# Kernel tuning notes

Hardware: AMD Instinct MI355X
Metric: run time of the kernel (lower is better)

## Reference

```python
import jax, jax.numpy as jnp
import numpy as np

EMBED = 1024
HEADS = 16

def setup_inputs() -> dict:
    key = jax.random.key(0)
    ks = jax.random.split(key, 6)
    N, S = 1, 4096
    half = EMBED // 2
    x = jax.random.normal(ks[0], (N, S, EMBED), dtype=jnp.float32)
    Wq = jax.random.normal(ks[1], (half, half), dtype=jnp.float32) * 0.02
    Wk = jax.random.normal(ks[2], (half, half), dtype=jnp.float32) * 0.02
    Wv = jax.random.normal(ks[3], (half, half), dtype=jnp.float32) * 0.02
    Wo = jax.random.normal(ks[4], (EMBED, half), dtype=jnp.float32) * 0.02
    bo = jnp.zeros((EMBED,), dtype=jnp.float32)
    return {"x": x, "Wq": Wq, "Wk": Wk, "Wv": Wv, "Wo": Wo, "bo": bo}

def reference(x, Wq, Wk, Wv, Wo, bo):
    N, S, E = x.shape
    H = HEADS
    Dh = (E // 2) // H                 # per-head dim of the half-width projections (32)
    scale = float(E // H) ** 0.5       # original scales by head_dim = embed/heads = 64
    left = x[..., : E // 2]            # only the left chunk feeds attention in the source
    # torch Linear: y = x @ W.T (no bias)
    q = (left @ Wq.T).reshape(N, S, H, Dh)
    k = (left @ Wk.T).reshape(N, S, H, Dh)
    v = (left @ Wv.T).reshape(N, S, H, Dh)
    energy = jnp.einsum('nqhd,nkhd->nqkh', q, k)          # [N,S,S,H] full score tensor
    att = jax.nn.softmax(energy / scale, axis=2)          # softmax over key axis
    out = jnp.einsum('nqkh,nkhd->nqhd', att, v)           # [N,S,H,Dh]
    out = out.reshape(N, S, E // 2)
    return out @ Wo.T + bo                                # fc_out: half -> embed
```

## Files before the change

kernel.cpp:

```cpp
#include <hip/hip_runtime.h>
#include <stdint.h>


#define SEQ    4096
#define DMODEL 1024
#define DHALF  512
#define NH     16
#define DH     32

typedef __attribute__((ext_vector_type(4))) float facc4;
typedef __attribute__((ext_vector_type(8))) short bfrag8;

#define MFMA_BF16(a, b, c) __builtin_amdgcn_mfma_f32_16x16x32_bf16((a), (b), (c), 0, 0, 0)

static __device__ __forceinline__ void gll16(const void* g, void* l) {
    typedef const __attribute__((address_space(1))) void GV;
    typedef __attribute__((address_space(3))) void LV;
    __builtin_amdgcn_global_load_lds((GV*)g, (LV*)l, 16, 0, 0);
}

static __device__ __forceinline__ uint16_t f2b(float x) {
    uint32_t u = __float_as_uint(x);
    return (uint16_t)((u + 0x7FFFu + ((u >> 16) & 1u)) >> 16);
}
static __device__ __forceinline__ float b2f(uint16_t b) {
    return __uint_as_float(((uint32_t)b) << 16);
}

static __device__ __forceinline__ bfrag8 cvt8perm(float4 a, float4 b) {
    uint32_t u0 = __float_as_uint(a.x) + 0x8000u, u1 = __float_as_uint(a.y) + 0x8000u;
    uint32_t u2 = __float_as_uint(a.z) + 0x8000u, u3 = __float_as_uint(a.w) + 0x8000u;
    uint32_t u4 = __float_as_uint(b.x) + 0x8000u, u5 = __float_as_uint(b.y) + 0x8000u;
    uint32_t u6 = __float_as_uint(b.z) + 0x8000u, u7 = __float_as_uint(b.w) + 0x8000u;
    union { uint32_t w[4]; bfrag8 r; } u;
    u.w[0] = __builtin_amdgcn_perm(u1, u0, 0x07060302u);
    u.w[1] = __builtin_amdgcn_perm(u3, u2, 0x07060302u);
    u.w[2] = __builtin_amdgcn_perm(u5, u4, 0x07060302u);
    u.w[3] = __builtin_amdgcn_perm(u7, u6, 0x07060302u);
    return u.r;
}

__global__ __launch_bounds__(256) void convert_w(
    const float* __restrict__ Wq, const float* __restrict__ Wk,
    const float* __restrict__ Wv, const float* __restrict__ Wo,
    const float* __restrict__ x,
    uint16_t* __restrict__ q, uint16_t* __restrict__ k,
    uint16_t* __restrict__ v, uint16_t* __restrict__ o,
    uint16_t* __restrict__ xb)
{
    int zz = blockIdx.x;
    if (zz >= 640) {
        size_t g = (size_t)(zz - 640) * 2048 + (size_t)threadIdx.x * 8;
        int row = (int)(g >> 9);
        int col = (int)(g & 511);
        const float* src = &x[(size_t)row * DMODEL + col];
        float4 a = *(const float4*)src;
        float4 b = *(const float4*)(src + 4);
        *(bfrag8*)&xb[g] = cvt8perm(a, b);
        return;
    }
    const float* src; uint16_t* dst; size_t off;
    if      (zz < 128) { src = Wq; dst = q; off = (size_t)zz * 2048; }
    else if (zz < 256) { src = Wk; dst = k; off = (size_t)(zz - 128) * 2048; }
    else if (zz < 384) { src = Wv; dst = v; off = (size_t)(zz - 256) * 2048; }
    else               { src = Wo; dst = o; off = (size_t)(zz - 384) * 2048; }
    size_t i = off + (size_t)threadIdx.x * 8;
    float4 a = *(const float4*)&src[i];
    float4 b = *(const float4*)&src[i + 4];
    *(bfrag8*)&dst[i] = cvt8perm(a, b);
}

__device__ __forceinline__ void gemm128(
    const uint16_t* __restrict__ A, int lda,
    const uint16_t* __restrict__ B, int ldb,
    void* __restrict__ C, int ldc, int cF32,
    const float* __restrict__ bias, float scale,
    int Kd, int m0, int n0)
{
    __shared__ __align__(16) uint16_t As[2][128 * 32];
    __shared__ __align__(16) uint16_t Bs[2][128 * 32];

    const int tid  = threadIdx.x;
    const int lane = tid & 63;
    const int wv   = tid >> 6;
    const int lo   = lane & 15;
    const int quad = lane >> 4;
    const int rb   = (wv >> 1) * 64;
    const int cb   = (wv & 1) * 64;

    const facc4 ZACC = {0.f, 0.f, 0.f, 0.f};
    facc4 acc[4][4];
#pragma unroll
    for (int i = 0; i < 4; ++i)
#pragma unroll
        for (int j = 0; j < 4; ++j) acc[i][j] = ZACC;

    const int lrow = lane >> 2;
    const int scol = (((lane & 3) ^ (lrow & 3)) << 3);
    const uint16_t* gA0 = &A[(size_t)(m0 + wv * 32 + lrow) * lda + scol];
    const uint16_t* gA1 = gA0 + (size_t)16 * lda;
    const uint16_t* gB0 = &B[(size_t)(n0 + wv * 32 + lrow) * ldb + scol];
    const uint16_t* gB1 = gB0 + (size_t)16 * ldb;
    const int d0 = wv * 1024;
    const int d1 = d0 + 512;

    const int rdo = lo * 32 + ((quad ^ (lo & 3)) << 3);

    gll16(gA0, &As[0][d0]); gll16(gA1, &As[0][d1]);
    gll16(gB0, &Bs[0][d0]); gll16(gB1, &Bs[0][d1]);
    __syncthreads();

    int p = 0;
    for (int kt = 0; kt < Kd; kt += 32) {
        const bool more = (kt + 32 < Kd);
        if (more) {
            gll16(gA0 + kt + 32, &As[1 - p][d0]); gll16(gA1 + kt + 32, &As[1 - p][d1]);
            gll16(gB0 + kt + 32, &Bs[1 - p][d0]); gll16(gB1 + kt + 32, &Bs[1 - p][d1]);
        }

        bfrag8 af[4], bf[4];
#pragma unroll
        for (int i = 0; i < 4; ++i) {
            af[i] = *(const bfrag8*)&As[p][rb * 32 + i * 512 + rdo];
            bf[i] = *(const bfrag8*)&Bs[p][cb * 32 + i * 512 + rdo];
        }
#pragma unroll
        for (int i = 0; i < 4; ++i)
#pragma unroll
            for (int j = 0; j < 4; ++j)
                acc[i][j] = MFMA_BF16(bf[j], af[i], acc[i][j]);

        if (more) {
            __syncthreads();
            p ^= 1;
        }
    }

#pragma unroll
    for (int i = 0; i < 4; ++i) {
        const size_t row = (size_t)(m0 + rb + i * 16 + lo);
#pragma unroll
        for (int j = 0; j < 4; ++j) {
            const int colb = n0 + cb + j * 16 + quad * 4;
            float4 bv = {0.f, 0.f, 0.f, 0.f};
            if (bias) bv = *(const float4*)&bias[colb];
            float v0 = acc[i][j][0] * scale + bv.x;
            float v1 = acc[i][j][1] * scale + bv.y;
            float v2 = acc[i][j][2] * scale + bv.z;
            float v3 = acc[i][j][3] * scale + bv.w;
            if (cF32) {
                float4 o = {v0, v1, v2, v3};
                *(float4*)&((float*)C)[row * ldc + colb] = o;
            } else {
                uint2 o;
                o.x = (uint32_t)f2b(v0) | ((uint32_t)f2b(v1) << 16);
                o.y = (uint32_t)f2b(v2) | ((uint32_t)f2b(v3) << 16);
                *(uint2*)&((uint16_t*)C)[row * ldc + colb] = o;
            }
        }
    }
}

#define SC_Q (0.125f * 1.4426950408889634f)

__global__ __launch_bounds__(256, 2) void qkv_kernel(
    const uint16_t* __restrict__ xb,
    const uint16_t* __restrict__ Wqb, const uint16_t* __restrict__ Wkb,
    const uint16_t* __restrict__ Wvb,
    uint16_t* __restrict__ Q, uint16_t* __restrict__ K, uint16_t* __restrict__ V)
{
    const int z = blockIdx.z;
    const uint16_t* W = (z == 0) ? Wqb : (z == 1) ? Wkb : Wvb;
    uint16_t* Out     = (z == 0) ? Q   : (z == 1) ? K   : V;
    float scale       = (z == 0) ? SC_Q : 1.0f;
    gemm128(xb, DHALF, W, DHALF, Out, DHALF, 0, nullptr, scale, DHALF,
            blockIdx.y * 128, blockIdx.x * 128);
}

__global__ __launch_bounds__(256, 2) void outproj_kernel(
    const uint16_t* __restrict__ O, const uint16_t* __restrict__ Wob,
    const float* __restrict__ bo, float* __restrict__ Y)
{
    gemm128(O, DHALF, Wob, DHALF, Y, DMODEL, 1, bo, 1.0f, DHALF,
            blockIdx.y * 128, blockIdx.x * 128);
}

__global__ __launch_bounds__(512) void attn_kernel(
    const uint16_t* __restrict__ Q, const uint16_t* __restrict__ Kb,
    const uint16_t* __restrict__ Vb, uint16_t* __restrict__ Op,
    float* __restrict__ lbuf, int kspan)
{
    __shared__ __align__(16) uint16_t Ks[2][128 * 40];
    __shared__ __align__(16) uint16_t Vt[2][32 * 128];

    const int tid  = threadIdx.x;
    const int lane = tid & 63;
    const int wv   = tid >> 6;
    const int lo   = lane & 15;
    const int quad = lane >> 4;

    const int f  = blockIdx.x + 16 * blockIdx.y + 256 * blockIdx.z;
    const int pp = (f & 7) | ((f >> 7) << 3);
    const int h  = pp & 15;
    const int sp = pp >> 4;
    const int q0 = ((f >> 3) & 15) * 256;

    const int srow = tid >> 2;
    const int skq  = (tid & 3) * 8;

    const facc4 ZACC = {0.f, 0.f, 0.f, 0.f};

    bfrag8 qf[2];
    qf[0] = *(const bfrag8*)&Q[(size_t)(q0 + wv * 32 + lo) * DHALF + h * DH + quad * 8];
    qf[1] = *(const bfrag8*)&Q[(size_t)(q0 + wv * 32 + 16 + lo) * DHALF + h * DH + quad * 8];

    bfrag8 ones;
#pragma unroll
    for (int j = 0; j < 8; ++j) ones[j] = (short)0x3F80;

    int vt_w[8];
    {
        int pb = ((srow >> 5) << 2) | ((srow >> 2) & 3);
        int pw = (((srow >> 4) & 1) << 2) | (srow & 3);
#pragma unroll
        for (int j = 0; j < 8; ++j) {
            int d  = skq + j;
            int Rd = ((d & 7) + 2 * (d >> 3)) & 7;
            vt_w[j] = d * 128 + (((pb + Rd) & 15) << 3) + pw;
        }
    }
    int vt_r[4][2];
#pragma unroll
    for (int dt = 0; dt < 2; ++dt) {
        int d  = dt * 16 + lo;
        int Rd = ((d & 7) + 2 * (d >> 3)) & 7;
#pragma unroll
        for (int c = 0; c < 4; ++c)
            vt_r[c][dt] = d * 128 + ((((c * 4 + quad) + Rd) & 15) << 3);
    }
    const int ks_r = lo * 40 + quad * 8;

    const uint16_t* kp = &Kb[(size_t)(sp * kspan + srow) * DHALF + h * DH + skq];
    const uint16_t* vp = &Vb[(size_t)(sp * kspan + srow) * DHALF + h * DH + skq];

    facc4 oacc[2][2], oaccL[2];
    oacc[0][0] = ZACC; oacc[0][1] = ZACC;
    oacc[1][0] = ZACC; oacc[1][1] = ZACC;
    oaccL[0] = ZACC; oaccL[1] = ZACC;

    float4 kreg = *(const float4*)kp;
    float4 vreg = *(const float4*)vp;
    kp += 128 * DHALF;
    vp += 128 * DHALF;

#define STAGE(BUF) do {                                                       \
        *(float4*)&Ks[BUF][srow * 40 + skq] = kreg;                           \
        const uint16_t* vsp = (const uint16_t*)&vreg;                         \
        _Pragma("unroll")                                                     \
        for (int j = 0; j < 8; ++j) Vt[BUF][vt_w[j]] = vsp[j];                \
    } while (0)

#define HALF(BUF, HH) do {                                                    \
        uint2 w0[4], w1[4];                                                   \
        _Pragma("unroll")                                                     \
        for (int t4 = 0; t4 < 4; ++t4) {                                      \
            bfrag8 kf = *(const bfrag8*)&Ks[BUF][(4 * HH + t4) * 640 + ks_r]; \
            facc4 s0 = MFMA_BF16(kf, qf[0], ZACC);                            \
            facc4 s1 = MFMA_BF16(kf, qf[1], ZACC);                            \
            uint32_t a0 = __float_as_uint(__builtin_amdgcn_exp2f(s0[0])) + 0x8000u; \
            uint32_t a1 = __float_as_uint(__builtin_amdgcn_exp2f(s0[1])) + 0x8000u; \
            uint32_t a2 = __float_as_uint(__builtin_amdgcn_exp2f(s0[2])) + 0x8000u; \
            uint32_t a3 = __float_as_uint(__builtin_amdgcn_exp2f(s0[3])) + 0x8000u; \
            w0[t4].x = __builtin_amdgcn_perm(a1, a0, 0x07060302u);            \
            w0[t4].y = __builtin_amdgcn_perm(a3, a2, 0x07060302u);            \
            uint32_t b0 = __float_as_uint(__builtin_amdgcn_exp2f(s1[0])) + 0x8000u; \
            uint32_t b1 = __float_as_uint(__builtin_amdgcn_exp2f(s1[1])) + 0x8000u; \
            uint32_t b2 = __float_as_uint(__builtin_amdgcn_exp2f(s1[2])) + 0x8000u; \
            uint32_t b3 = __float_as_uint(__builtin_amdgcn_exp2f(s1[3])) + 0x8000u; \
            w1[t4].x = __builtin_amdgcn_perm(b1, b0, 0x07060302u);            \
            w1[t4].y = __builtin_amdgcn_perm(b3, b2, 0x07060302u);            \
        }                                                                     \
        union PU { uint2 u2[2]; bfrag8 f; } pu;                               \
        bfrag8 pf0[2], pf1[2];                                                \
        pu.u2[0] = w0[0]; pu.u2[1] = w0[1]; pf0[0] = pu.f;                    \
        pu.u2[0] = w0[2]; pu.u2[1] = w0[3]; pf0[1] = pu.f;                    \
        pu.u2[0] = w1[0]; pu.u2[1] = w1[1]; pf1[0] = pu.f;                    \
        pu.u2[0] = w1[2]; pu.u2[1] = w1[3]; pf1[1] = pu.f;                    \
        _Pragma("unroll")                                                     \
        for (int cc = 0; cc < 2; ++cc) {                                      \
            _Pragma("unroll")                                                 \
            for (int dt = 0; dt < 2; ++dt) {                                  \
                bfrag8 vf = *(const bfrag8*)&Vt[BUF][vt_r[2 * HH + cc][dt]];  \
                oacc[0][dt] = MFMA_BF16(pf0[cc], vf, oacc[0][dt]);            \
                oacc[1][dt] = MFMA_BF16(pf1[cc], vf, oacc[1][dt]);            \
            }                                                                 \
            oaccL[0] = MFMA_BF16(pf0[cc], ones, oaccL[0]);                    \
            oaccL[1] = MFMA_BF16(pf1[cc], ones, oaccL[1]);                    \
        }                                                                     \
    } while (0)

#define TILE(BUF) do { HALF(BUF, 0); HALF(BUF, 1); } while (0)

    STAGE(0);
    __syncthreads();

    const int nt = kspan >> 7;
    for (int t = 0; t < nt; t += 2) {
        kreg = *(const float4*)kp;
        vreg = *(const float4*)vp;
        kp += 128 * DHALF; vp += 128 * DHALF;
        TILE(0);
        STAGE(1);
        __syncthreads();

        const bool more = (t + 2 < nt);
        if (more) {
            kreg = *(const float4*)kp;
            vreg = *(const float4*)vp;
            kp += 128 * DHALF; vp += 128 * DHALF;
        }
        TILE(1);
        if (more) {
            STAGE(0);
            __syncthreads();
        }
    }
#undef STAGE
#undef HALF
#undef TILE

    if (lo == 0) {
#pragma unroll
        for (int g = 0; g < 2; ++g)
#pragma unroll
            for (int r = 0; r < 4; ++r)
                lbuf[((size_t)sp * NH + h) * SEQ + q0 + wv * 32 + g * 16 + quad * 4 + r] =
                    oaccL[g][r];
    }

    uint16_t* Od = Op + (size_t)sp * SEQ * DHALF;
#pragma unroll
    for (int g = 0; g < 2; ++g) {
#pragma unroll
        for (int r = 0; r < 4; ++r) {
            int row = q0 + wv * 32 + g * 16 + quad * 4 + r;
            Od[(size_t)row * DHALF + h * DH + lo]      = f2b(oacc[g][0][r]);
            Od[(size_t)row * DHALF + h * DH + 16 + lo] = f2b(oacc[g][1][r]);
        }
    }
}

__global__ __launch_bounds__(256) void combine_kernel(
    const uint16_t* __restrict__ Op, const float* __restrict__ lbuf,
    uint16_t* __restrict__ O, int ns)
{
    int t   = blockIdx.x * 256 + threadIdx.x;
    int row = t >> 6;
    int cb  = (t & 63) << 3;
    int h   = cb >> 5;
    float l = 0.f;
    float acc[8] = {0.f, 0.f, 0.f, 0.f, 0.f, 0.f, 0.f, 0.f};
    for (int sp = 0; sp < ns; ++sp) {
        l += lbuf[((size_t)sp * NH + h) * SEQ + row];
        bfrag8 a = *(const bfrag8*)&Op[(size_t)sp * SEQ * DHALF + (size_t)row * DHALF + cb];
#pragma unroll
        for (int j = 0; j < 8; ++j) acc[j] += b2f((uint16_t)a[j]);
    }
    float inv = 1.0f / l;
    bfrag8 o;
#pragma unroll
    for (int j = 0; j < 8; ++j) o[j] = (short)f2b(acc[j] * inv);
    *(bfrag8*)&O[(size_t)row * DHALF + cb] = o;
}

extern "C" void kernel_launch(void* const* d_in, const int* in_sizes, int n_in,
                              void* d_out, int out_size, void* d_ws, size_t ws_size,
                              hipStream_t stream)
{
    const float* x  = (const float*)d_in[0];
    const float* Wq = (const float*)d_in[1];
    const float* Wk = (const float*)d_in[2];
    const float* Wv = (const float*)d_in[3];
    const float* Wo = (const float*)d_in[4];
    const float* bo = (const float*)d_in[5];

    const int ns = 2;

    uint16_t* Wqb = (uint16_t*)d_ws;
    uint16_t* Wkb = Wqb + (size_t)DHALF * DHALF;
    uint16_t* Wvb = Wkb + (size_t)DHALF * DHALF;
    uint16_t* Wob = Wvb + (size_t)DHALF * DHALF;
    uint16_t* Q   = Wob + (size_t)DMODEL * DHALF;
    uint16_t* K   = Q + (size_t)SEQ * DHALF;
    uint16_t* V   = K + (size_t)SEQ * DHALF;
    uint16_t* O   = V + (size_t)SEQ * DHALF;
    uint16_t* Op  = O + (size_t)SEQ * DHALF;
    float*  lbuf  = (float*)(Op + (size_t)ns * SEQ * DHALF);
    uint16_t* xb  = O;

    convert_w<<<1664, 256, 0, stream>>>(Wq, Wk, Wv, Wo, x, Wqb, Wkb, Wvb, Wob, xb);
    qkv_kernel<<<dim3(DHALF / 128, SEQ / 128, 3), 256, 0, stream>>>(
        xb, Wqb, Wkb, Wvb, Q, K, V);
    attn_kernel<<<dim3(SEQ / 256, NH, ns), 512, 0, stream>>>(Q, K, V, Op, lbuf, SEQ / ns);
    combine_kernel<<<1024, 256, 0, stream>>>(Op, lbuf, O, ns);
    outproj_kernel<<<dim3(DMODEL / 128, SEQ / 128), 256, 0, stream>>>(
        O, Wob, bo, (float*)d_out);
}
```

Baseline: 161.0 us.

## Fuse split-combine into out-projection, merge QKV weights, shrink GEMM tiles

```diff
diff --git a/kernel.cpp b/kernel.cpp
--- a/kernel.cpp
+++ b/kernel.cpp
@@ -7,6 +7,7 @@
 #define DHALF  512
 #define NH     16
 #define DH     32
+#define LDQ    1536
 
 typedef __attribute__((ext_vector_type(4))) float facc4;
 typedef __attribute__((ext_vector_type(8))) short bfrag8;
@@ -40,12 +41,13 @@
     return u.r;
 }
 
+#define SC_Q (0.125f * 1.4426950408889634f)
+
 __global__ __launch_bounds__(256) void convert_w(
     const float* __restrict__ Wq, const float* __restrict__ Wk,
     const float* __restrict__ Wv, const float* __restrict__ Wo,
     const float* __restrict__ x,
-    uint16_t* __restrict__ q, uint16_t* __restrict__ k,
-    uint16_t* __restrict__ v, uint16_t* __restrict__ o,
+    uint16_t* __restrict__ wqkv, uint16_t* __restrict__ wo,
     uint16_t* __restrict__ xb)
 {
     int zz = blockIdx.x;
@@ -59,25 +61,24 @@
         *(bfrag8*)&xb[g] = cvt8perm(a, b);
         return;
     }
-    const float* src; uint16_t* dst; size_t off;
-    if      (zz < 128) { src = Wq; dst = q; off = (size_t)zz * 2048; }
-    else if (zz < 256) { src = Wk; dst = k; off = (size_t)(zz - 128) * 2048; }
-    else if (zz < 384) { src = Wv; dst = v; off = (size_t)(zz - 256) * 2048; }
-    else               { src = Wo; dst = o; off = (size_t)(zz - 384) * 2048; }
+    const float* src; uint16_t* dst; size_t off; float sc = 1.0f;
+    if      (zz < 128) { src = Wq; dst = wqkv;          off = (size_t)zz * 2048; sc = SC_Q; }
+    else if (zz < 256) { src = Wk; dst = wqkv + 262144; off = (size_t)(zz - 128) * 2048; }
+    else if (zz < 384) { src = Wv; dst = wqkv + 524288; off = (size_t)(zz - 256) * 2048; }
+    else               { src = Wo; dst = wo;            off = (size_t)(zz - 384) * 2048; }
     size_t i = off + (size_t)threadIdx.x * 8;
     float4 a = *(const float4*)&src[i];
     float4 b = *(const float4*)&src[i + 4];
+    a.x *= sc; a.y *= sc; a.z *= sc; a.w *= sc;
+    b.x *= sc; b.y *= sc; b.z *= sc; b.w *= sc;
     *(bfrag8*)&dst[i] = cvt8perm(a, b);
 }
 
-__device__ __forceinline__ void gemm128(
-    const uint16_t* __restrict__ A, int lda,
-    const uint16_t* __restrict__ B, int ldb,
-    void* __restrict__ C, int ldc, int cF32,
-    const float* __restrict__ bias, float scale,
-    int Kd, int m0, int n0)
+__global__ __launch_bounds__(256) void qkv_kernel(
+    const uint16_t* __restrict__ xb, const uint16_t* __restrict__ Wqkv,
+    uint16_t* __restrict__ QKV)
 {
-    __shared__ __align__(16) uint16_t As[2][128 * 32];
+    __shared__ __align__(16) uint16_t As[2][64 * 32];
     __shared__ __align__(16) uint16_t Bs[2][128 * 32];
 
     const int tid  = threadIdx.x;
@@ -85,47 +86,49 @@
     const int wv   = tid >> 6;
     const int lo   = lane & 15;
     const int quad = lane >> 4;
-    const int rb   = (wv >> 1) * 64;
-    const int cb   = (wv & 1) * 64;
+    const int m0   = blockIdx.y * 64;
+    const int n0   = blockIdx.x * 128;
+    const int rt   = (wv >> 1) * 32;
+    const int ct   = (wv & 1) * 64;
 
     const facc4 ZACC = {0.f, 0.f, 0.f, 0.f};
-    facc4 acc[4][4];
-#pragma unroll
-    for (int i = 0; i < 4; ++i)
+    facc4 acc[2][4];
+#pragma unroll
+    for (int i = 0; i < 2; ++i)
 #pragma unroll
         for (int j = 0; j < 4; ++j) acc[i][j] = ZACC;
 
     const int lrow = lane >> 2;
     const int scol = (((lane & 3) ^ (lrow & 3)) << 3);
-    const uint16_t* gA0 = &A[(size_t)(m0 + wv * 32 + lrow) * lda + scol];
-    const uint16_t* gA1 = gA0 + (size_t)16 * lda;
-    const uint16_t* gB0 = &B[(size_t)(n0 + wv * 32 + lrow) * ldb + scol];
-    const uint16_t* gB1 = gB0 + (size_t)16 * ldb;
-    const int d0 = wv * 1024;
-    const int d1 = d0 + 512;
-
+    const uint16_t* gA  = &xb[(size_t)(m0 + wv * 16 + lrow) * DHALF + scol];
+    const uint16_t* gB0 = &Wqkv[(size_t)(n0 + wv * 32 + lrow) * DHALF + scol];
+    const uint16_t* gB1 = gB0 + (size_t)16 * DHALF;
+    const int dA  = wv * 512;
+    const int dB0 = wv * 1024, dB1 = dB0 + 512;
     const int rdo = lo * 32 + ((quad ^ (lo & 3)) << 3);
 
-    gll16(gA0, &As[0][d0]); gll16(gA1, &As[0][d1]);
-    gll16(gB0, &Bs[0][d0]); gll16(gB1, &Bs[0][d1]);
+    gll16(gA, &As[0][dA]);
+    gll16(gB0, &Bs[0][dB0]); gll16(gB1, &Bs[0][dB1]);
     __syncthreads();
 
     int p = 0;
-    for (int kt = 0; kt < Kd; kt += 32) {
-        const bool more = (kt + 32 < Kd);
-        if (more) {
-            gll16(gA0 + kt + 32, &As[1 - p][d0]); gll16(gA1 + kt + 32, &As[1 - p][d1]);
-            gll16(gB0 + kt + 32, &Bs[1 - p][d0]); gll16(gB1 + kt + 32, &Bs[1 - p][d1]);
-        }
-
-        bfrag8 af[4], bf[4];
-#pragma unroll
-        for (int i = 0; i < 4; ++i) {
-            af[i] = *(const bfrag8*)&As[p][rb * 32 + i * 512 + rdo];
-            bf[i] = *(const bfrag8*)&Bs[p][cb * 32 + i * 512 + rdo];
-        }
-#pragma unroll
-        for (int i = 0; i < 4; ++i)
+    for (int kt = 0; kt < DHALF; kt += 32) {
+        const bool more = (kt + 32 < DHALF);
+        if (more) {
+            gll16(gA + kt + 32, &As[1 - p][dA]);
+            gll16(gB0 + kt + 32, &Bs[1 - p][dB0]);
+            gll16(gB1 + kt + 32, &Bs[1 - p][dB1]);
+        }
+
+        bfrag8 af[2], bf[4];
+#pragma unroll
+        for (int i = 0; i < 2; ++i)
+            af[i] = *(const bfrag8*)&As[p][rt * 32 + i * 512 + rdo];
+#pragma unroll
+        for (int j = 0; j < 4; ++j)
+            bf[j] = *(const bfrag8*)&Bs[p][ct * 32 + j * 512 + rdo];
+#pragma unroll
+        for (int i = 0; i < 2; ++i)
 #pragma unroll
             for (int j = 0; j < 4; ++j)
                 acc[i][j] = MFMA_BF16(bf[j], af[i], acc[i][j]);
@@ -137,67 +140,142 @@
     }
 
 #pragma unroll
-    for (int i = 0; i < 4; ++i) {
-        const size_t row = (size_t)(m0 + rb + i * 16 + lo);
+    for (int i = 0; i < 2; ++i) {
+        const size_t row = (size_t)(m0 + rt + i * 16 + lo);
 #pragma unroll
         for (int j = 0; j < 4; ++j) {
-            const int colb = n0 + cb + j * 16 + quad * 4;
-            float4 bv = {0.f, 0.f, 0.f, 0.f};
-            if (bias) bv = *(const float4*)&bias[colb];
-            float v0 = acc[i][j][0] * scale + bv.x;
-            float v1 = acc[i][j][1] * scale + bv.y;
-            float v2 = acc[i][j][2] * scale + bv.z;
-            float v3 = acc[i][j][3] * scale + bv.w;
-            if (cF32) {
-                float4 o = {v0, v1, v2, v3};
-                *(float4*)&((float*)C)[row * ldc + colb] = o;
-            } else {
-                uint2 o;
-                o.x = (uint32_t)f2b(v0) | ((uint32_t)f2b(v1) << 16);
-                o.y = (uint32_t)f2b(v2) | ((uint32_t)f2b(v3) << 16);
-                *(uint2*)&((uint16_t*)C)[row * ldc + colb] = o;
-            }
-        }
-    }
-}
-
-#define SC_Q (0.125f * 1.4426950408889634f)
-
-__global__ __launch_bounds__(256, 2) void qkv_kernel(
-    const uint16_t* __restrict__ xb,
-    const uint16_t* __restrict__ Wqb, const uint16_t* __restrict__ Wkb,
-    const uint16_t* __restrict__ Wvb,
-    uint16_t* __restrict__ Q, uint16_t* __restrict__ K, uint16_t* __restrict__ V)
+            const int colb = n0 + ct + j * 16 + quad * 4;
+            uint2 o;
+            o.x = (uint32_t)f2b(acc[i][j][0]) | ((uint32_t)f2b(acc[i][j][1]) << 16);
+            o.y = (uint32_t)f2b(acc[i][j][2]) | ((uint32_t)f2b(acc[i][j][3]) << 16);
+            *(uint2*)&QKV[row * LDQ + colb] = o;
+        }
+    }
+}
+
+__global__ __launch_bounds__(256) void outproj_kernel(
+    const uint16_t* __restrict__ Op, const float* __restrict__ lbuf,
+    const uint16_t* __restrict__ Wob, const float* __restrict__ bo,
+    float* __restrict__ Y)
 {
-    const int z = blockIdx.z;
-    const uint16_t* W = (z == 0) ? Wqb : (z == 1) ? Wkb : Wvb;
-    uint16_t* Out     = (z == 0) ? Q   : (z == 1) ? K   : V;
-    float scale       = (z == 0) ? SC_Q : 1.0f;
-    gemm128(xb, DHALF, W, DHALF, Out, DHALF, 0, nullptr, scale, DHALF,
-            blockIdx.y * 128, blockIdx.x * 128);
-}
-
-__global__ __launch_bounds__(256, 2) void outproj_kernel(
-    const uint16_t* __restrict__ O, const uint16_t* __restrict__ Wob,
-    const float* __restrict__ bo, float* __restrict__ Y)
-{
-    gemm128(O, DHALF, Wob, DHALF, Y, DMODEL, 1, bo, 1.0f, DHALF,
-            blockIdx.y * 128, blockIdx.x * 128);
-}
-
-__global__ __launch_bounds__(512) void attn_kernel(
-    const uint16_t* __restrict__ Q, const uint16_t* __restrict__ Kb,
-    const uint16_t* __restrict__ Vb, uint16_t* __restrict__ Op,
-    float* __restrict__ lbuf, int kspan)
-{
-    __shared__ __align__(16) uint16_t Ks[2][128 * 40];
-    __shared__ __align__(16) uint16_t Vt[2][32 * 128];
+    __shared__ __align__(16) uint16_t As[2][64 * 32];
+    __shared__ __align__(16) uint16_t Bs[2][128 * 32];
 
     const int tid  = threadIdx.x;
     const int lane = tid & 63;
     const int wv   = tid >> 6;
     const int lo   = lane & 15;
     const int quad = lane >> 4;
+    const int m0   = blockIdx.y * 64;
+    const int n0   = blockIdx.x * 128;
+    const int rt   = (wv >> 1) * 32;
+    const int ct   = (wv & 1) * 64;
+
+    const facc4 ZACC = {0.f, 0.f, 0.f, 0.f};
+    facc4 acc[2][4];
+#pragma unroll
+    for (int i = 0; i < 2; ++i)
+#pragma unroll
+        for (int j = 0; j < 4; ++j) acc[i][j] = ZACC;
+
+    const int lrow = lane >> 2;
+    const int scol = (((lane & 3) ^ (lrow & 3)) << 3);
+    const int arow = m0 + wv * 16 + lrow;
+    const uint16_t* gO0 = &Op[(size_t)arow * DHALF + scol];
+    const uint16_t* gO1 = gO0 + (size_t)SEQ * DHALF;
+    const float* lb0 = &lbuf[arow];
+    const float* lb1 = &lbuf[(size_t)NH * SEQ + arow];
+    const uint16_t* gB0 = &Wob[(size_t)(n0 + wv * 32 + lrow) * DHALF + scol];
+    const uint16_t* gB1 = gB0 + (size_t)16 * DHALF;
+    const int dA  = wv * 512 + lane * 8;
+    const int dB0 = wv * 1024, dB1 = dB0 + 512;
+    const int rdo = lo * 32 + ((quad ^ (lo & 3)) << 3);
+
+#define PACKA(A0, A1, INV)                                                    \
+    ({ float4 fa_, fb_;                                                       \
+       fa_.x = (b2f((uint16_t)(A0)[0]) + b2f((uint16_t)(A1)[0])) * (INV);     \
+       fa_.y = (b2f((uint16_t)(A0)[1]) + b2f((uint16_t)(A1)[1])) * (INV);     \
+       fa_.z = (b2f((uint16_t)(A0)[2]) + b2f((uint16_t)(A1)[2])) * (INV);     \
+       fa_.w = (b2f((uint16_t)(A0)[3]) + b2f((uint16_t)(A1)[3])) * (INV);     \
+       fb_.x = (b2f((uint16_t)(A0)[4]) + b2f((uint16_t)(A1)[4])) * (INV);     \
+       fb_.y = (b2f((uint16_t)(A0)[5]) + b2f((uint16_t)(A1)[5])) * (INV);     \
+       fb_.z = (b2f((uint16_t)(A0)[6]) + b2f((uint16_t)(A1)[6])) * (INV);     \
+       fb_.w = (b2f((uint16_t)(A0)[7]) + b2f((uint16_t)(A1)[7])) * (INV);     \
+       cvt8perm(fa_, fb_); })
+
+    {
+        bfrag8 a0 = *(const bfrag8*)gO0;
+        bfrag8 a1 = *(const bfrag8*)gO1;
+        float inv = 1.0f / (lb0[0] + lb1[0]);
+        *(bfrag8*)&As[0][dA] = PACKA(a0, a1, inv);
+        gll16(gB0, &Bs[0][dB0]); gll16(gB1, &Bs[0][dB1]);
+    }
+    __syncthreads();
+
+    int p = 0;
+    for (int kt = 0; kt < DHALF; kt += 32) {
+        const bool more = (kt + 32 < DHALF);
+        bfrag8 na0, na1; float nl = 1.0f;
+        if (more) {
+            na0 = *(const bfrag8*)(gO0 + kt + 32);
+            na1 = *(const bfrag8*)(gO1 + kt + 32);
+            const int hh = (kt + 32) >> 5;
+            nl = lb0[(size_t)hh * SEQ] + lb1[(size_t)hh * SEQ];
+            gll16(gB0 + kt + 32, &Bs[1 - p][dB0]);
+            gll16(gB1 + kt + 32, &Bs[1 - p][dB1]);
+        }
+
+        bfrag8 af[2], bf[4];
+#pragma unroll
+        for (int i = 0; i < 2; ++i)
+            af[i] = *(const bfrag8*)&As[p][rt * 32 + i * 512 + rdo];
+#pragma unroll
+        for (int j = 0; j < 4; ++j)
+            bf[j] = *(const bfrag8*)&Bs[p][ct * 32 + j * 512 + rdo];
+#pragma unroll
+        for (int i = 0; i < 2; ++i)
+#pragma unroll
+            for (int j = 0; j < 4; ++j)
+                acc[i][j] = MFMA_BF16(bf[j], af[i], acc[i][j]);
+
+        if (more) {
+            float inv = 1.0f / nl;
+            *(bfrag8*)&As[1 - p][dA] = PACKA(na0, na1, inv);
+            __syncthreads();
+            p ^= 1;
+        }
+    }
+#undef PACKA
+
+#pragma unroll
+    for (int i = 0; i < 2; ++i) {
+        const size_t row = (size_t)(m0 + rt + i * 16 + lo);
+#pragma unroll
+        for (int j = 0; j < 4; ++j) {
+            const int colb = n0 + ct + j * 16 + quad * 4;
+            float4 bv = *(const float4*)&bo[colb];
+            float4 o;
+            o.x = acc[i][j][0] + bv.x;
+            o.y = acc[i][j][1] + bv.y;
+            o.z = acc[i][j][2] + bv.z;
+            o.w = acc[i][j][3] + bv.w;
+            *(float4*)&Y[row * DMODEL + colb] = o;
+        }
+    }
+}
+
+__global__ __launch_bounds__(512) void attn_kernel(
+    const uint16_t* __restrict__ QKV, uint16_t* __restrict__ Op,
+    float* __restrict__ lbuf, int kspan)
+{
+    __shared__ __align__(16) uint16_t Ks[2][128 * 40];
+    __shared__ __align__(16) uint16_t Vt[2][32 * 128];
+
+    const int tid  = threadIdx.x;
+    const int lane = tid & 63;
+    const int wv   = tid >> 6;
+    const int lo   = lane & 15;
+    const int quad = lane >> 4;
 
     const int f  = blockIdx.x + 16 * blockIdx.y + 256 * blockIdx.z;
     const int pp = (f & 7) | ((f >> 7) << 3);
@@ -211,8 +289,8 @@
     const facc4 ZACC = {0.f, 0.f, 0.f, 0.f};
 
     bfrag8 qf[2];
-    qf[0] = *(const bfrag8*)&Q[(size_t)(q0 + wv * 32 + lo) * DHALF + h * DH + quad * 8];
-    qf[1] = *(const bfrag8*)&Q[(size_t)(q0 + wv * 32 + 16 + lo) * DHALF + h * DH + quad * 8];
+    qf[0] = *(const bfrag8*)&QKV[(size_t)(q0 + wv * 32 + lo) * LDQ + h * DH + quad * 8];
+    qf[1] = *(const bfrag8*)&QKV[(size_t)(q0 + wv * 32 + 16 + lo) * LDQ + h * DH + quad * 8];
 
     bfrag8 ones;
 #pragma unroll
@@ -240,8 +318,8 @@
     }
     const int ks_r = lo * 40 + quad * 8;
 
-    const uint16_t* kp = &Kb[(size_t)(sp * kspan + srow) * DHALF + h * DH + skq];
-    const uint16_t* vp = &Vb[(size_t)(sp * kspan + srow) * DHALF + h * DH + skq];
+    const uint16_t* kp = &QKV[(size_t)(sp * kspan + srow) * LDQ + DHALF + h * DH + skq];
+    const uint16_t* vp = &QKV[(size_t)(sp * kspan + srow) * LDQ + 2 * DHALF + h * DH + skq];
 
     facc4 oacc[2][2], oaccL[2];
     oacc[0][0] = ZACC; oacc[0][1] = ZACC;
@@ -250,8 +328,8 @@
 
     float4 kreg = *(const float4*)kp;
     float4 vreg = *(const float4*)vp;
-    kp += 128 * DHALF;
-    vp += 128 * DHALF;
+    kp += (size_t)128 * LDQ;
+    vp += (size_t)128 * LDQ;
 
 #define STAGE(BUF) do {                                                       \
         *(float4*)&Ks[BUF][srow * 40 + skq] = kreg;                           \
@@ -308,7 +386,7 @@
     for (int t = 0; t < nt; t += 2) {
         kreg = *(const float4*)kp;
         vreg = *(const float4*)vp;
-        kp += 128 * DHALF; vp += 128 * DHALF;
+        kp += (size_t)128 * LDQ; vp += (size_t)128 * LDQ;
         TILE(0);
         STAGE(1);
         __syncthreads();
@@ -317,7 +395,7 @@
         if (more) {
             kreg = *(const float4*)kp;
             vreg = *(const float4*)vp;
-            kp += 128 * DHALF; vp += 128 * DHALF;
+            kp += (size_t)128 * LDQ; vp += (size_t)128 * LDQ;
         }
         TILE(1);
         if (more) {
@@ -348,29 +426,6 @@
             Od[(size_t)row * DHALF + h * DH + 16 + lo] = f2b(oacc[g][1][r]);
         }
     }
-}
-
-__global__ __launch_bounds__(256) void combine_kernel(
-    const uint16_t* __restrict__ Op, const float* __restrict__ lbuf,
-    uint16_t* __restrict__ O, int ns)
-{
-    int t   = blockIdx.x * 256 + threadIdx.x;
-    int row = t >> 6;
-    int cb  = (t & 63) << 3;
-    int h   = cb >> 5;
-    float l = 0.f;
-    float acc[8] = {0.f, 0.f, 0.f, 0.f, 0.f, 0.f, 0.f, 0.f};
-    for (int sp = 0; sp < ns; ++sp) {
-        l += lbuf[((size_t)sp * NH + h) * SEQ + row];
-        bfrag8 a = *(const bfrag8*)&Op[(size_t)sp * SEQ * DHALF + (size_t)row * DHALF + cb];
-#pragma unroll
-        for (int j = 0; j < 8; ++j) acc[j] += b2f((uint16_t)a[j]);
-    }
-    float inv = 1.0f / l;
-    bfrag8 o;
-#pragma unroll
-    for (int j = 0; j < 8; ++j) o[j] = (short)f2b(acc[j] * inv);
-    *(bfrag8*)&O[(size_t)row * DHALF + cb] = o;
 }
 
 extern "C" void kernel_launch(void* const* d_in, const int* in_sizes, int n_in,
@@ -384,25 +439,16 @@
     const float* Wo = (const float*)d_in[4];
     const float* bo = (const float*)d_in[5];
 
-    const int ns = 2;
-
-    uint16_t* Wqb = (uint16_t*)d_ws;
-    uint16_t* Wkb = Wqb + (size_t)DHALF * DHALF;
-    uint16_t* Wvb = Wkb + (size_t)DHALF * DHALF;
-    uint16_t* Wob = Wvb + (size_t)DHALF * DHALF;
-    uint16_t* Q   = Wob + (size_t)DMODEL * DHALF;
-    uint16_t* K   = Q + (size_t)SEQ * DHALF;
-    uint16_t* V   = K + (size_t)SEQ * DHALF;
-    uint16_t* O   = V + (size_t)SEQ * DHALF;
-    uint16_t* Op  = O + (size_t)SEQ * DHALF;
-    float*  lbuf  = (float*)(Op + (size_t)ns * SEQ * DHALF);
-    uint16_t* xb  = O;
-
-    convert_w<<<1664, 256, 0, stream>>>(Wq, Wk, Wv, Wo, x, Wqb, Wkb, Wvb, Wob, xb);
-    qkv_kernel<<<dim3(DHALF / 128, SEQ / 128, 3), 256, 0, stream>>>(
-        xb, Wqb, Wkb, Wvb, Q, K, V);
-    attn_kernel<<<dim3(SEQ / 256, NH, ns), 512, 0, stream>>>(Q, K, V, Op, lbuf, SEQ / ns);
-    combine_kernel<<<1024, 256, 0, stream>>>(Op, lbuf, O, ns);
-    outproj_kernel<<<dim3(DMODEL / 128, SEQ / 128), 256, 0, stream>>>(
-        O, Wob, bo, (float*)d_out);
-}
+    uint16_t* Wqkv = (uint16_t*)d_ws;
+    uint16_t* Wob  = Wqkv + 786432;
+    uint16_t* QKV  = Wob + 524288;
+    uint16_t* Op   = QKV + (size_t)SEQ * LDQ;
+    float*  lbuf   = (float*)(Op + (size_t)2 * SEQ * DHALF);
+    uint16_t* xb   = Op;
+
+    convert_w<<<1664, 256, 0, stream>>>(Wq, Wk, Wv, Wo, x, Wqkv, Wob, xb);
+    qkv_kernel<<<dim3(LDQ / 128, SEQ / 64), 256, 0, stream>>>(xb, Wqkv, QKV);
+    attn_kernel<<<dim3(SEQ / 256, NH, 2), 512, 0, stream>>>(QKV, Op, lbuf, SEQ / 2);
+    outproj_kernel<<<dim3(DMODEL / 128, SEQ / 64), 256, 0, stream>>>(
+        Op, lbuf, Wob, bo, (float*)d_out);
+}
```

Result: slower. 169.8 us (+5.5%).

## Fuse x fp32-to-bf16 conversion into QKV GEMM and raise attention key splits

Applied to the files above, without the earlier changes.

```diff
diff --git a/kernel.cpp b/kernel.cpp
--- a/kernel.cpp
+++ b/kernel.cpp
@@ -43,22 +43,10 @@
 __global__ __launch_bounds__(256) void convert_w(
     const float* __restrict__ Wq, const float* __restrict__ Wk,
     const float* __restrict__ Wv, const float* __restrict__ Wo,
-    const float* __restrict__ x,
     uint16_t* __restrict__ q, uint16_t* __restrict__ k,
-    uint16_t* __restrict__ v, uint16_t* __restrict__ o,
-    uint16_t* __restrict__ xb)
+    uint16_t* __restrict__ v, uint16_t* __restrict__ o)
 {
     int zz = blockIdx.x;
-    if (zz >= 640) {
-        size_t g = (size_t)(zz - 640) * 2048 + (size_t)threadIdx.x * 8;
-        int row = (int)(g >> 9);
-        int col = (int)(g & 511);
-        const float* src = &x[(size_t)row * DMODEL + col];
-        float4 a = *(const float4*)src;
-        float4 b = *(const float4*)(src + 4);
-        *(bfrag8*)&xb[g] = cvt8perm(a, b);
-        return;
-    }
     const float* src; uint16_t* dst; size_t off;
     if      (zz < 128) { src = Wq; dst = q; off = (size_t)zz * 2048; }
     else if (zz < 256) { src = Wk; dst = k; off = (size_t)(zz - 128) * 2048; }
@@ -70,6 +58,103 @@
     *(bfrag8*)&dst[i] = cvt8perm(a, b);
 }
 
+#define SC_Q (0.125f * 1.4426950408889634f)
+
+__global__ __launch_bounds__(256, 2) void qkv_kernel(
+    const float* __restrict__ x,
+    const uint16_t* __restrict__ Wqb, const uint16_t* __restrict__ Wkb,
+    const uint16_t* __restrict__ Wvb,
+    uint16_t* __restrict__ Q, uint16_t* __restrict__ K, uint16_t* __restrict__ V)
+{
+    __shared__ __align__(16) uint16_t As[2][128 * 40];
+    __shared__ __align__(16) uint16_t Bs[2][128 * 32];
+
+    const int z = blockIdx.z;
+    const uint16_t* W = (z == 0) ? Wqb : (z == 1) ? Wkb : Wvb;
+    uint16_t* Out     = (z == 0) ? Q   : (z == 1) ? K   : V;
+    const float scale = (z == 0) ? SC_Q : 1.0f;
+    const int m0 = blockIdx.y * 128;
+    const int n0 = blockIdx.x * 128;
+
+    const int tid  = threadIdx.x;
+    const int lane = tid & 63;
+    const int wv   = tid >> 6;
+    const int lo   = lane & 15;
+    const int quad = lane >> 4;
+    const int srow = tid >> 2;
+    const int skq  = (tid & 3) * 8;
+    const int rb   = (wv >> 1) * 64;
+    const int cb   = (wv & 1) * 64;
+
+    const facc4 ZACC = {0.f, 0.f, 0.f, 0.f};
+    facc4 acc[4][4];
+#pragma unroll
+    for (int i = 0; i < 4; ++i)
+#pragma unroll
+        for (int j = 0; j < 4; ++j) acc[i][j] = ZACC;
+
+    const float* fA0 = &x[(size_t)(m0 + srow) * DMODEL + skq];
+    const float* fA1 = &x[(size_t)(m0 + srow + 64) * DMODEL + skq];
+
+    const int lrow = lane >> 2;
+    const int scol = (((lane & 3) ^ (lrow & 3)) << 3);
+    const uint16_t* gB0 = &W[(size_t)(n0 + wv * 32 + lrow) * DHALF + scol];
+    const uint16_t* gB1 = gB0 + (size_t)16 * DHALF;
+    const int dB0 = wv * 1024, dB1 = dB0 + 512;
+    const int rdo = lo * 32 + ((quad ^ (lo & 3)) << 3);
+
+    float4 f0a = *(const float4*)fA0, f0b = *(const float4*)(fA0 + 4);
+    float4 f1a = *(const float4*)fA1, f1b = *(const float4*)(fA1 + 4);
+
+    *(bfrag8*)&As[0][srow * 40 + skq]        = cvt8perm(f0a, f0b);
+    *(bfrag8*)&As[0][(srow + 64) * 40 + skq] = cvt8perm(f1a, f1b);
+    gll16(gB0, &Bs[0][dB0]); gll16(gB1, &Bs[0][dB1]);
+    __syncthreads();
+
+    int p = 0;
+    for (int kt = 0; kt < DHALF; kt += 32) {
+        const bool more = (kt + 32 < DHALF);
+        if (more) {
+            f0a = *(const float4*)(fA0 + kt + 32); f0b = *(const float4*)(fA0 + kt + 36);
+            f1a = *(const float4*)(fA1 + kt + 32); f1b = *(const float4*)(fA1 + kt + 36);
+            gll16(gB0 + kt + 32, &Bs[1 - p][dB0]);
+            gll16(gB1 + kt + 32, &Bs[1 - p][dB1]);
+        }
+
+        bfrag8 af[4], bf[4];
+#pragma unroll
+        for (int i = 0; i < 4; ++i) {
+            af[i] = *(const bfrag8*)&As[p][(rb + i * 16 + lo) * 40 + quad * 8];
+            bf[i] = *(const bfrag8*)&Bs[p][cb * 32 + i * 512 + rdo];
+        }
+#pragma unroll
+        for (int i = 0; i < 4; ++i)
+#pragma unroll
+            for (int j = 0; j < 4; ++j)
+                acc[i][j] = MFMA_BF16(bf[j], af[i], acc[i][j]);
+
+        if (more) {
+            *(bfrag8*)&As[1 - p][srow * 40 + skq]        = cvt8perm(f0a, f0b);
+            *(bfrag8*)&As[1 - p][(srow + 64) * 40 + skq] = cvt8perm(f1a, f1b);
+            __syncthreads();
+            p ^= 1;
+        }
+    }
+
+#pragma unroll
+    for (int i = 0; i < 4; ++i) {
+        const size_t row = (size_t)(m0 + rb + i * 16 + lo);
+#pragma unroll
+        for (int j = 0; j < 4; ++j) {
+            const int colb = n0 + cb + j * 16 + quad * 4;
+            uint2 o;
+            o.x = (uint32_t)f2b(acc[i][j][0] * scale) | ((uint32_t)f2b(acc[i][j][1] * scale) << 16);
+            o.y = (uint32_t)f2b(acc[i][j][2] * scale) | ((uint32_t)f2b(acc[i][j][3] * scale) << 16);
+            *(uint2*)&Out[row * DHALF + colb] = o;
+        }
+    }
+}
+
 __device__ __forceinline__ void gemm128(
     const uint16_t* __restrict__ A, int lda,
     const uint16_t* __restrict__ B, int ldb,
@@ -103,7 +188,6 @@
     const uint16_t* gB1 = gB0 + (size_t)16 * ldb;
     const int d0 = wv * 1024;
     const int d1 = d0 + 512;
-
     const int rdo = lo * 32 + ((quad ^ (lo & 3)) << 3);
 
     gll16(gA0, &As[0][d0]); gll16(gA1, &As[0][d1]);
@@ -159,22 +243,6 @@
             }
         }
     }
-}
-
-#define SC_Q (0.125f * 1.4426950408889634f)
-
-__global__ __launch_bounds__(256, 2) void qkv_kernel(
-    const uint16_t* __restrict__ xb,
-    const uint16_t* __restrict__ Wqb, const uint16_t* __restrict__ Wkb,
-    const uint16_t* __restrict__ Wvb,
-    uint16_t* __restrict__ Q, uint16_t* __restrict__ K, uint16_t* __restrict__ V)
-{
-    const int z = blockIdx.z;
-    const uint16_t* W = (z == 0) ? Wqb : (z == 1) ? Wkb : Wvb;
-    uint16_t* Out     = (z == 0) ? Q   : (z == 1) ? K   : V;
-    float scale       = (z == 0) ? SC_Q : 1.0f;
-    gemm128(xb, DHALF, W, DHALF, Out, DHALF, 0, nullptr, scale, DHALF,
-            blockIdx.y * 128, blockIdx.x * 128);
 }
 
 __global__ __launch_bounds__(256, 2) void outproj_kernel(
@@ -384,7 +452,11 @@
     const float* Wo = (const float*)d_in[4];
     const float* bo = (const float*)d_in[5];
 
-    const int ns = 2;
+    size_t fixed_e = 3 * (size_t)DHALF * DHALF + (size_t)DMODEL * DHALF
+                   + 4 * (size_t)SEQ * DHALF;
+    size_t need4 = (fixed_e + 4 * (size_t)SEQ * DHALF) * 2
+                 + 4 * (size_t)NH * SEQ * 4;
+    const int ns = (ws_size >= need4) ? 4 : 2;
 
     uint16_t* Wqb = (uint16_t*)d_ws;
     uint16_t* Wkb = Wqb + (size_t)DHALF * DHALF;
@@ -396,11 +468,10 @@
     uint16_t* O   = V + (size_t)SEQ * DHALF;
     uint16_t* Op  = O + (size_t)SEQ * DHALF;
     float*  lbuf  = (float*)(Op + (size_t)ns * SEQ * DHALF);
-    uint16_t* xb  = O;
-
-    convert_w<<<1664, 256, 0, stream>>>(Wq, Wk, Wv, Wo, x, Wqb, Wkb, Wvb, Wob, xb);
+
+    convert_w<<<640, 256, 0, stream>>>(Wq, Wk, Wv, Wo, Wqb, Wkb, Wvb, Wob);
     qkv_kernel<<<dim3(DHALF / 128, SEQ / 128, 3), 256, 0, stream>>>(
-        xb, Wqb, Wkb, Wvb, Q, K, V);
+        x, Wqb, Wkb, Wvb, Q, K, V);
     attn_kernel<<<dim3(SEQ / 256, NH, ns), 512, 0, stream>>>(Q, K, V, Op, lbuf, SEQ / ns);
     combine_kernel<<<1024, 256, 0, stream>>>(Op, lbuf, O, ns);
     outproj_kernel<<<dim3(DMODEL / 128, SEQ / 128), 256, 0, stream>>>(
```

After: 171.1 us. +6.3%, slower.
